# Kernel optimization log

Measured on AMD Instinct MI355X. Metric: run time of the kernel, lower is better.

The kernel has to match this reference:

```python
import jax, jax.numpy as jnp
import numpy as np

B, T, H, N = 4, 2048, 512, 8
THETA = 10000.0
PERIOD, RET_ORDER = 3, 2  # num_inputs, mgdt ret_order


def setup_inputs() -> dict:
    key = jax.random.key(0)
    ks = jax.random.split(key, 9)
    s = 0.02
    return {
        "x": jax.random.normal(ks[0], (B, T, H), dtype=jnp.float32),
        "Wq": jax.random.normal(ks[1], (H, H), dtype=jnp.float32) * s,
        "bq": jax.random.normal(ks[2], (H,), dtype=jnp.float32) * s,
        "Wk": jax.random.normal(ks[3], (H, H), dtype=jnp.float32) * s,
        "bk": jax.random.normal(ks[4], (H,), dtype=jnp.float32) * s,
        "Wv": jax.random.normal(ks[5], (H, H), dtype=jnp.float32) * s,
        "bv": jax.random.normal(ks[6], (H,), dtype=jnp.float32) * s,
        "Wo": jax.random.normal(ks[7], (H, H), dtype=jnp.float32) * s,
        "bo": jax.random.normal(ks[8], (H,), dtype=jnp.float32) * s,
    }


def _rope(z, cos, sin):
    # RoPE over the FULL hidden dim (applied before head split, as in source)
    b, t, c = z.shape
    z = z.reshape(b, t, c // 2, 2)
    zr = z[..., 0] * cos - z[..., 1] * sin
    zi = z[..., 0] * sin + z[..., 1] * cos
    return jnp.stack([zr, zi], axis=-1).reshape(b, t, c)


def reference(x, Wq, bq, Wk, bk, Wv, bv, Wo, bo):
    Bx, Tx, C = x.shape
    D = C // N

    # precomputed freqs_cis -> cos/sin, shape (T, C//2)
    inv_freq = 1.0 / (THETA ** (jnp.arange(0, C, 2, dtype=jnp.float32) / C))
    ang = jnp.arange(Tx, dtype=jnp.float32)[:, None] * inv_freq[None, :]
    cos, sin = jnp.cos(ang), jnp.sin(ang)

    q = x @ Wq + bq
    k = x @ Wk + bk
    q = _rope(q, cos, sin)
    k = _rope(k, cos, sin)
    v = x @ Wv + bv

    # (B, N, T, D)
    q = q.reshape(Bx, Tx, N, D).transpose(0, 2, 1, 3)
    k = k.reshape(Bx, Tx, N, D).transpose(0, 2, 1, 3)
    v = v.reshape(Bx, Tx, N, D).transpose(0, 2, 1, 3)

    scores = jnp.einsum("bntd,bnsd->bnts", q, k) / jnp.float32(D) ** 0.5

    # causal tril mask with mgdt column masking (cols period+ret_order-1, step period)
    mask = jnp.tril(jnp.ones((Tx, Tx), dtype=bool))
    ret_cols = np.arange(PERIOD + RET_ORDER - 1, Tx, PERIOD)
    mask = mask.at[:, ret_cols].set(False)

    scores = jnp.where(mask[None, None], scores, -jnp.inf)
    att = jax.nn.softmax(scores, axis=-1)  # (B,N,T,T)

    out = jnp.einsum("bnts,bnsd->bntd", att, v)
    out = out.transpose(0, 2, 1, 3).reshape(Bx, Tx, C)
    return out @ Wo + bo
```

## Files before the change

kernel.cpp:

```cpp
#include <hip/hip_runtime.h>

typedef unsigned short u16;
typedef __attribute__((ext_vector_type(8))) short bf16x8;
typedef __attribute__((ext_vector_type(8))) unsigned short u16x8;
typedef __attribute__((ext_vector_type(4))) float f32x4;
typedef __attribute__((ext_vector_type(16))) float f32x16;
typedef __attribute__((ext_vector_type(4))) unsigned int u32x4;

#define MFMA16(a, b, c) __builtin_amdgcn_mfma_f32_16x16x32_bf16((a), (b), (c), 0, 0, 0)
#define MFMA32(a, b, c) __builtin_amdgcn_mfma_f32_32x32x16_bf16((a), (b), (c), 0, 0, 0)

static constexpr int CB = 4, CT = 2048, CH = 512, CN = 8, CD = 64;
static constexpr int CM = CB * CT;

__device__ __forceinline__ u16 f2bf(float f) {
    union { float f; unsigned int i; } v; v.f = f;
    unsigned int r = v.i + 0x7FFFu + ((v.i >> 16) & 1u);
    return (u16)(r >> 16);
}

__device__ __forceinline__ int kc_of(int t) {
    return t + 1 - ((t >= 4) ? ((t - 1) / 3) : 0);
}

__device__ __forceinline__ void gl16(const u16* g, u16* l) {
    __builtin_amdgcn_global_load_lds(
        (const __attribute__((address_space(1))) void*)g,
        (__attribute__((address_space(3))) void*)l, 16, 0, 0);
}


__global__ void cvt_x_kernel(const float* __restrict__ x, u16* __restrict__ xb, int n4) {
    int i = blockIdx.x * blockDim.x + threadIdx.x;
    const float4* x4 = (const float4*)x;
    for (; i < n4; i += gridDim.x * blockDim.x) {
        float4 v = x4[i];
        unsigned long long pack = (unsigned long long)f2bf(v.x)
                                | ((unsigned long long)f2bf(v.y) << 16)
                                | ((unsigned long long)f2bf(v.z) << 32)
                                | ((unsigned long long)f2bf(v.w) << 48);
        ((unsigned long long*)xb)[i] = pack;
    }
}

__global__ void wt_kernel(const float* __restrict__ Wq, const float* __restrict__ Wk,
                          const float* __restrict__ Wv, const float* __restrict__ Wo,
                          u16* __restrict__ Wt) {
    __shared__ float tile[32][33];
    const float* W = (blockIdx.z == 0) ? Wq : (blockIdx.z == 1) ? Wk
                   : (blockIdx.z == 2) ? Wv : Wo;
    u16* dst = Wt + (size_t)blockIdx.z * CH * CH;
    int n0 = blockIdx.x * 32, k0 = blockIdx.y * 32;
    int tx = threadIdx.x, ty = threadIdx.y;
    for (int j = 0; j < 32; j += 8)
        tile[ty + j][tx] = W[(size_t)(k0 + ty + j) * CH + n0 + tx];
    __syncthreads();
    for (int j = 0; j < 32; j += 8)
        dst[(size_t)(n0 + ty + j) * CH + k0 + tx] = f2bf(tile[tx][ty + j]);
}

__global__ void rope_tab_kernel(float2* __restrict__ tab) {
    int i = blockIdx.x * blockDim.x + threadIdx.x;
    if (i >= CT * (CH / 2)) return;
    int t = i >> 8, h = i & 255;
    float inv = exp2f(-(float)h * (13.287712379549449f / 256.0f));
    float ang = (float)t * inv;
    float s, c;
    sincosf(ang, &s, &c);
    tab[i] = make_float2(c, s);
}


__device__ __forceinline__ void gemm_bt_main(const u16* __restrict__ A, const u16* __restrict__ Bt,
                                             int m0, int n0, f32x4 acc[4][2]) {
    __shared__ __align__(16) u16 Al[128 * 32];
    __shared__ __align__(16) u16 Bl[128 * 32];
    const int tid = threadIdx.x;
    const int lane = tid & 63;
    const int w = tid >> 6;
    const int wm = w >> 2, wn = w & 3;
    const int lg = lane >> 4, lr = lane & 15;

    const int srow = w * 16 + (lane >> 2);
    const int schunk = ((lane & 3) ^ ((lane >> 3) & 3)) * 8;
    const u16* ga = A  + (size_t)(m0 + srow) * CH + schunk;
    const u16* gb = Bt + (size_t)(n0 + srow) * CH + schunk;
    u16* lA0 = Al + w * 512;
    u16* lB0 = Bl + w * 512;

    const int rchunk = (lg ^ ((lr >> 1) & 3)) * 8;

    for (int k0 = 0; k0 < CH; k0 += 32) {
        __syncthreads();
        gl16(ga + k0, lA0);
        gl16(gb + k0, lB0);
        __syncthreads();
        bf16x8 af[4], bfr[2];
#pragma unroll
        for (int i = 0; i < 4; ++i)
            af[i] = *(const bf16x8*)(Al + (wm * 64 + i * 16 + lr) * 32 + rchunk);
#pragma unroll
        for (int i = 0; i < 2; ++i)
            bfr[i] = *(const bf16x8*)(Bl + (wn * 32 + i * 16 + lr) * 32 + rchunk);
#pragma unroll
        for (int mi = 0; mi < 4; ++mi)
#pragma unroll
            for (int ni = 0; ni < 2; ++ni)
                acc[mi][ni] = MFMA16(af[mi], bfr[ni], acc[mi][ni]);
    }
}

__global__ __launch_bounds__(512) void gemm_qkv_kernel(
    const u16* __restrict__ xb, const u16* __restrict__ Wt,
    const float* __restrict__ bq, const float* __restrict__ bk, const float* __restrict__ bv,
    const float2* __restrict__ tab,
    u16* __restrict__ q_ws, u16* __restrict__ k_ws, u16* __restrict__ v_t) {
    f32x4 acc[4][2];
#pragma unroll
    for (int mi = 0; mi < 4; ++mi)
#pragma unroll
        for (int ni = 0; ni < 2; ++ni)
#pragma unroll
            for (int e = 0; e < 4; ++e) acc[mi][ni][e] = 0.f;

    const int m0 = blockIdx.x * 128, n0 = blockIdx.y * 128;
    gemm_bt_main(xb, Wt, m0, n0, acc);

    const int lane = threadIdx.x & 63;
    const int w = threadIdx.x >> 6, wm = w >> 2, wn = w & 3;
    const int lg = lane >> 4, lr = lane & 15;
    const int seg = n0 >> 9;
    const float* bias_p = (seg == 0) ? bq : (seg == 1) ? bk : bv;

#pragma unroll
    for (int ni = 0; ni < 2; ++ni) {
        const int c = n0 + wn * 32 + ni * 16 + lr;
        const int cc = c & 511;
        const int nh = cc >> 6, d = cc & 63;
        const float bias = bias_p[cc];
#pragma unroll
        for (int mi = 0; mi < 4; ++mi) {
#pragma unroll
            for (int r = 0; r < 4; ++r) {
                const int row = m0 + wm * 64 + mi * 16 + lg * 4 + r;
                const int b = row >> 11, t = row & 2047;
                float val = acc[mi][ni][r] + bias;
                if (seg < 2) {
                    float2 cs = tab[t * 256 + (cc >> 1)];
                    float partner = __shfl_xor(val, 1);
                    val = val * cs.x + ((lane & 1) ? partner * cs.y : -partner * cs.y);
                }
                if (seg == 0) {
                    val *= 0.18033688011112f;
                    q_ws[(size_t)((b * CN + nh) * CT + t) * CD + d] = f2bf(val);
                } else {
                    const bool msk = (t >= 4) && (t % 3 == 1);
                    if (!msk) {
                        const int ci = t - ((t >= 4) ? ((t - 1) / 3) : 0);
                        const int tile = ci >> 5, sl = ci & 31;
                        const size_t tb = (size_t)(b * CN + nh) * CT * CD + (size_t)tile * 2048;
                        if (seg == 1) {
                            const int cF = d >> 4, hF = (d >> 3) & 1, jF = d & 7;
                            k_ws[tb + ((cF * 2 + hF) * 32 + sl) * 8 + jF] = f2bf(val);
                        } else {
                            const int kbF = sl >> 4, hF = (sl >> 3) & 1, jF = sl & 7;
                            const int dhF = d >> 5, qlF = d & 31;
                            v_t[tb + (((dhF * 2 + kbF) * 2 + hF) * 32 + qlF) * 8 + jF] = f2bf(val);
                        }
                    }
                }
            }
        }
    }
}

__global__ __launch_bounds__(512) void gemm_out_kernel(
    const u16* __restrict__ att, const u16* __restrict__ Wot,
    const float* __restrict__ bo, float* __restrict__ out) {
    f32x4 acc[4][2];
#pragma unroll
    for (int mi = 0; mi < 4; ++mi)
#pragma unroll
        for (int ni = 0; ni < 2; ++ni)
#pragma unroll
            for (int e = 0; e < 4; ++e) acc[mi][ni][e] = 0.f;

    const int m0 = blockIdx.x * 128, n0 = blockIdx.y * 128;
    gemm_bt_main(att, Wot, m0, n0, acc);

    const int lane = threadIdx.x & 63;
    const int w = threadIdx.x >> 6, wm = w >> 2, wn = w & 3;
    const int lg = lane >> 4, lr = lane & 15;
#pragma unroll
    for (int ni = 0; ni < 2; ++ni) {
        const int c = n0 + wn * 32 + ni * 16 + lr;
        const float bias = bo[c];
#pragma unroll
        for (int mi = 0; mi < 4; ++mi)
#pragma unroll
            for (int r = 0; r < 4; ++r) {
                const int row = m0 + wm * 64 + mi * 16 + lg * 4 + r;
                out[(size_t)row * CH + c] = acc[mi][ni][r] + bias;
            }
    }
}

__global__ __launch_bounds__(256, 4) void attn_kernel(
    const u16* __restrict__ q_ws, const u16* __restrict__ k_ws,
    const u16* __restrict__ v_t, u16* __restrict__ attout) {
    const int bid = blockIdx.x;
    const int xcd = bid & 7, idx = bid >> 3;
    const int bn = xcd + 8 * (idx >> 6);
    const int qb = 63 - (idx & 63);
    const int q0 = qb * 32;
    const int l = threadIdx.x & 63;
    const int w = threadIdx.x >> 6;
    const int ql = l & 31, h = l >> 5;

    const int t = q0 + ql;
    const int kct = kc_of(t);
    const int kcq0 = kc_of(q0);
    const int kcmax = kc_of(q0 + 31);
    const int ntc32 = (kcmax + 31) >> 5;

    const size_t baseq = (size_t)bn * CT * CD;
    const size_t basek = (size_t)bn * CT * CD;
    const size_t basev = (size_t)bn * CD * CT;

    bf16x8 qf[4];
    {
        const u16* qp = q_ws + baseq + (size_t)t * CD + h * 8;
#pragma unroll
        for (int c = 0; c < 4; ++c) qf[c] = *(const bf16x8*)(qp + c * 16);
    }

    f32x16 oa[2];
#pragma unroll
    for (int dh = 0; dh < 2; ++dh)
#pragma unroll
        for (int e = 0; e < 16; ++e) oa[dh][e] = 0.f;
    float lsum = 0.f;

    for (int i32 = w; i32 < ntc32; i32 += 4) {
        const int s0h = i32 * 32;
        const bool needmask = (s0h + 31 >= kcq0);
        const u16* ktile = k_ws + basek + (size_t)i32 * 2048;
        const u16* vtile = v_t + basev + (size_t)i32 * 2048;

        f32x16 sa;
#pragma unroll
        for (int e = 0; e < 16; ++e) sa[e] = 0.f;
#pragma unroll
        for (int c = 0; c < 4; ++c) {
            bf16x8 kf = *(const bf16x8*)(ktile + ((c * 2 + h) * 32 + ql) * 8);
            sa = MFMA32(kf, qf[c], sa);
        }

        float pr[16];
        if (needmask) {
#pragma unroll
            for (int g = 0; g < 16; ++g) {
                const int roff = (g & 3) + 8 * (g >> 2);
                float e = __builtin_amdgcn_exp2f(sa[g]);
                e = (s0h + roff + 4 * h < kct) ? e : 0.f;
                lsum += e;
                pr[g] = e;
            }
        } else {
#pragma unroll
            for (int g = 0; g < 16; ++g) {
                float e = __builtin_amdgcn_exp2f(sa[g]);
                lsum += e;
                pr[g] = e;
            }
        }

#pragma unroll
        for (int kb = 0; kb < 2; ++kb) {
            const int g0 = kb * 8;
            unsigned int w0, w1, w2, w3;
            asm("v_cvt_pk_bf16_f32 %0, %1, %2" : "=v"(w0) : "v"(pr[g0 + 0]), "v"(pr[g0 + 1]));
            asm("v_cvt_pk_bf16_f32 %0, %1, %2" : "=v"(w1) : "v"(pr[g0 + 2]), "v"(pr[g0 + 3]));
            asm("v_cvt_pk_bf16_f32 %0, %1, %2" : "=v"(w2) : "v"(pr[g0 + 4]), "v"(pr[g0 + 5]));
            asm("v_cvt_pk_bf16_f32 %0, %1, %2" : "=v"(w3) : "v"(pr[g0 + 6]), "v"(pr[g0 + 7]));
            const unsigned int x0 = (unsigned int)__shfl_xor((int)w0, 32);
            const unsigned int x1 = (unsigned int)__shfl_xor((int)w1, 32);
            const unsigned int x2 = (unsigned int)__shfl_xor((int)w2, 32);
            const unsigned int x3 = (unsigned int)__shfl_xor((int)w3, 32);
            u32x4 fw;
            fw.x = h ? x2 : w0;
            fw.y = h ? x3 : w1;
            fw.z = h ? w2 : x0;
            fw.w = h ? w3 : x1;
            const bf16x8 pa = __builtin_bit_cast(bf16x8, fw);
#pragma unroll
            for (int dh = 0; dh < 2; ++dh) {
                bf16x8 vf = *(const bf16x8*)(vtile + (((dh * 2 + kb) * 2 + h) * 32 + ql) * 8);
                oa[dh] = MFMA32(pa, vf, oa[dh]);
            }
        }
    }

    __shared__ float buf[2][64][33];
    __shared__ float lsp[4][64];
    __shared__ float lsf[32];

    lsp[w][l] = lsum;
    if (w >= 2) {
#pragma unroll
        for (int dh = 0; dh < 2; ++dh)
#pragma unroll
            for (int g = 0; g < 16; ++g)
                buf[w - 2][l][dh * 16 + g] = oa[dh][g];
    }
    __syncthreads();
    if (w < 2) {
#pragma unroll
        for (int dh = 0; dh < 2; ++dh)
#pragma unroll
            for (int g = 0; g < 16; ++g)
                oa[dh][g] += buf[w][l][dh * 16 + g];
    }
    if (threadIdx.x < 32) {
        const int r = threadIdx.x;
        float s = 0.f;
#pragma unroll
        for (int ww = 0; ww < 4; ++ww) s += lsp[ww][r] + lsp[ww][r + 32];
        lsf[r] = 1.f / s;
    }
    __syncthreads();
    if (w == 1) {
#pragma unroll
        for (int dh = 0; dh < 2; ++dh)
#pragma unroll
            for (int g = 0; g < 16; ++g)
                buf[0][l][dh * 16 + g] = oa[dh][g];
    }
    __syncthreads();
    if (w == 0) {
        const int b = bn >> 3, nh = bn & 7;
#pragma unroll
        for (int dh = 0; dh < 2; ++dh)
#pragma unroll
            for (int g = 0; g < 16; ++g) {
                const float s = oa[dh][g] + buf[0][l][dh * 16 + g];
                const int r = (g & 3) + 8 * (g >> 2) + 4 * h;
                attout[(size_t)(b * CT + q0 + r) * CH + nh * 64 + dh * 32 + ql] = f2bf(s * lsf[r]);
            }
    }
}


extern "C" void kernel_launch(void* const* d_in, const int* in_sizes, int n_in,
                              void* d_out, int out_size, void* d_ws, size_t ws_size,
                              hipStream_t stream) {
    const float* x  = (const float*)d_in[0];
    const float* Wq = (const float*)d_in[1];
    const float* bq = (const float*)d_in[2];
    const float* Wk = (const float*)d_in[3];
    const float* bk = (const float*)d_in[4];
    const float* Wv = (const float*)d_in[5];
    const float* bv = (const float*)d_in[6];
    const float* Wo = (const float*)d_in[7];
    const float* bo = (const float*)d_in[8];
    float* out = (float*)d_out;

    char* p = (char*)d_ws;
    u16* xb = (u16*)p;        p += (size_t)CM * CH * 2;
    u16* Wt = (u16*)p;        p += (size_t)4 * CH * CH * 2;
    float2* tab = (float2*)p; p += (size_t)CT * (CH / 2) * 8;
    u16* q_ws = (u16*)p;      p += (size_t)CM * CH * 2;
    u16* k_ws = (u16*)p;      p += (size_t)CM * CH * 2;
    u16* v_t  = (u16*)p;      p += (size_t)CM * CH * 2;
    u16* attout = (u16*)p;    p += (size_t)CM * CH * 2;

    cvt_x_kernel<<<2048, 256, 0, stream>>>(x, xb, CM * CH / 4);
    wt_kernel<<<dim3(16, 16, 4), dim3(32, 8), 0, stream>>>(Wq, Wk, Wv, Wo, Wt);
    rope_tab_kernel<<<dim3((CT * (CH / 2)) / 256), 256, 0, stream>>>(tab);
    gemm_qkv_kernel<<<dim3(CM / 128, (3 * CH) / 128), 512, 0, stream>>>(
        xb, Wt, bq, bk, bv, tab, q_ws, k_ws, v_t);
    attn_kernel<<<dim3(2048), 256, 0, stream>>>(q_ws, k_ws, v_t, attout);
    gemm_out_kernel<<<dim3(CM / 128, CH / 128), 512, 0, stream>>>(
        attout, Wt + (size_t)3 * CH * CH, bo, out);
}
```

Measured before the change: 85.36 us.

## Double-buffer LDS tiles in shared GEMM main loop to overlap loads with MFMA

Converts the bf16 GEMM main loop to ping-pong LDS buffers. The next K-slice is issued via gl16 direct-to-LDS loads before the MFMAs on the current slice run, and a single waitcnt plus barrier follows each step. This is meant to hide global-to-LDS latency behind compute and to halve the barriers per iteration. It doubles LDS use per block, which may reduce occupancy. It also relies on the manual vmcnt wait being enough for the LDS writes to be visible before the next reads.

```diff
diff --git a/kernel.cpp b/kernel.cpp
--- a/kernel.cpp
+++ b/kernel.cpp
@@ -73,8 +73,8 @@
 
 __device__ __forceinline__ void gemm_bt_main(const u16* __restrict__ A, const u16* __restrict__ Bt,
                                              int m0, int n0, f32x4 acc[4][2]) {
-    __shared__ __align__(16) u16 Al[128 * 32];
-    __shared__ __align__(16) u16 Bl[128 * 32];
+    __shared__ __align__(16) u16 Al[2][128 * 32];
+    __shared__ __align__(16) u16 Bl[2][128 * 32];
     const int tid = threadIdx.x;
     const int lane = tid & 63;
     const int w = tid >> 6;
@@ -85,28 +85,45 @@
     const int schunk = ((lane & 3) ^ ((lane >> 3) & 3)) * 8;
     const u16* ga = A  + (size_t)(m0 + srow) * CH + schunk;
     const u16* gb = Bt + (size_t)(n0 + srow) * CH + schunk;
-    u16* lA0 = Al + w * 512;
-    u16* lB0 = Bl + w * 512;
 
     const int rchunk = (lg ^ ((lr >> 1) & 3)) * 8;
 
+    gl16(ga, &Al[0][w * 512]);
+    gl16(gb, &Bl[0][w * 512]);
+    asm volatile("s_waitcnt vmcnt(0)" ::: "memory");
+    __builtin_amdgcn_s_barrier();
+    __builtin_amdgcn_sched_barrier(0);
+
+    int cur = 0;
+#pragma unroll 1
     for (int k0 = 0; k0 < CH; k0 += 32) {
-        __syncthreads();
-        gl16(ga + k0, lA0);
-        gl16(gb + k0, lB0);
-        __syncthreads();
+        if (k0 + 32 < CH) {
+            gl16(ga + k0 + 32, &Al[cur ^ 1][w * 512]);
+            gl16(gb + k0 + 32, &Bl[cur ^ 1][w * 512]);
+        }
+        __builtin_amdgcn_sched_barrier(0);
+
+        const u16* al = &Al[cur][0];
+        const u16* bl = &Bl[cur][0];
         bf16x8 af[4], bfr[2];
 #pragma unroll
         for (int i = 0; i < 4; ++i)
-            af[i] = *(const bf16x8*)(Al + (wm * 64 + i * 16 + lr) * 32 + rchunk);
+            af[i] = *(const bf16x8*)(al + (wm * 64 + i * 16 + lr) * 32 + rchunk);
 #pragma unroll
         for (int i = 0; i < 2; ++i)
-            bfr[i] = *(const bf16x8*)(Bl + (wn * 32 + i * 16 + lr) * 32 + rchunk);
+            bfr[i] = *(const bf16x8*)(bl + (wn * 32 + i * 16 + lr) * 32 + rchunk);
 #pragma unroll
         for (int mi = 0; mi < 4; ++mi)
 #pragma unroll
             for (int ni = 0; ni < 2; ++ni)
                 acc[mi][ni] = MFMA16(af[mi], bfr[ni], acc[mi][ni]);
+
+        if (k0 + 32 < CH) {
+            asm volatile("s_waitcnt vmcnt(0)" ::: "memory");
+            __builtin_amdgcn_s_barrier();
+            __builtin_amdgcn_sched_barrier(0);
+        }
+        cur ^= 1;
     }
 }
 
```

Measured after the change: 86.22 us. Within noise of the previous version (+1.0%).
